# Performance work log

Measured on AMD Instinct MI355X. Metric: run time of the kernel, lower is better.

The kernel has to match this reference:

```python
import jax, jax.numpy as jnp
import numpy as np

NUM_HEADS = 32
NUM_KV_HEADS = 8
HEAD_DIM = 128
SCALE = 1.0 / float(np.sqrt(128.0))
LENS = [1024, 896, 768, 512]          # variable sequence lengths (batch=4)
MAX_SEQLEN = 1024
NUM_SLOTS = 16384                      # 64 blocks * block_size 256
NEG_INF = -1e30


def setup_inputs() -> dict:
    key = jax.random.key(0)
    k0, k1, k2 = jax.random.split(key, 3)
    total = int(sum(LENS))
    q = jax.random.normal(k0, (total, NUM_HEADS, HEAD_DIM), dtype=jnp.float32)
    k = jax.random.normal(k1, (total, NUM_KV_HEADS, HEAD_DIM), dtype=jnp.float32)
    v = jax.random.normal(k2, (total, NUM_KV_HEADS, HEAD_DIM), dtype=jnp.float32)
    k_cache = jnp.zeros((NUM_SLOTS, NUM_KV_HEADS, HEAD_DIM), dtype=jnp.float32)
    v_cache = jnp.zeros((NUM_SLOTS, NUM_KV_HEADS, HEAD_DIM), dtype=jnp.float32)
    slot_mapping = jnp.arange(total, dtype=jnp.int32)
    cu = jnp.concatenate([jnp.zeros((1,), jnp.int32),
                          jnp.cumsum(jnp.array(LENS, dtype=jnp.int32))])
    return {"q": q, "k": k, "v": v, "k_cache": k_cache, "v_cache": v_cache,
            "slot_mapping": slot_mapping, "cu_seqlens_q": cu, "cu_seqlens_k": cu,
            "max_seqlen": MAX_SEQLEN}


def _varlen_prefill_attention(q, k, v, cu_q, cu_k, max_seqlen):
    # q: [T, H, D]; k, v: [T, Hkv, D]; packed variable-length sequences.
    total = q.shape[0]
    B = cu_q.shape[0] - 1
    G = NUM_HEADS // NUM_KV_HEADS  # GQA group size
    lens_q = cu_q[1:] - cu_q[:-1]
    lens_k = cu_k[1:] - cu_k[:-1]
    pos = jnp.arange(max_seqlen)[None, :]                     # [1, S]
    q_idx = jnp.clip(cu_q[:-1, None] + pos, 0, total - 1)     # [B, S]
    k_idx = jnp.clip(cu_k[:-1, None] + pos, 0, total - 1)
    q_valid = pos < lens_q[:, None]                           # [B, S]
    k_valid = pos < lens_k[:, None]
    # Gather into padded [B, S, heads, D] and zero the padding.
    qp = jnp.where(q_valid[:, :, None, None], q[q_idx], 0)
    kp = jnp.where(k_valid[:, :, None, None], k[k_idx], 0)
    vp = jnp.where(k_valid[:, :, None, None], v[k_idx], 0)
    qp = qp.reshape(B, max_seqlen, NUM_KV_HEADS, G, HEAD_DIM)
    # logits: [B, Hkv, G, Sq, Sk]
    logits = jnp.einsum('bqhgd,bkhd->bhgqk', qp, kp) * SCALE
    causal = jnp.arange(max_seqlen)[:, None] >= jnp.arange(max_seqlen)[None, :]
    full_mask = causal[None, :, :] & q_valid[:, :, None] & k_valid[:, None, :]  # [B,Sq,Sk]
    logits = jnp.where(full_mask[:, None, None, :, :], logits, NEG_INF)
    probs = jax.nn.softmax(logits, axis=-1)
    outp = jnp.einsum('bhgqk,bkhd->bqhgd', probs, vp)
    outp = outp.reshape(B, max_seqlen, NUM_HEADS, HEAD_DIM)
    # Scatter padded output back to packed layout.
    dest = q_idx.reshape(-1)
    out_flat = jnp.where(q_valid.reshape(-1)[:, None, None],
                         outp.reshape(-1, NUM_HEADS, HEAD_DIM), 0)
    out = jnp.zeros((total, NUM_HEADS, HEAD_DIM), dtype=q.dtype)
    out = out.at[dest].add(out_flat)
    return out


def reference(q, k, v, k_cache, v_cache, slot_mapping, cu_seqlens_q, cu_seqlens_k, max_seqlen):
    # store_kv_to_cache (scatter into paged cache)
    valid = slot_mapping >= 0
    safe = jnp.where(valid, slot_mapping, 0)
    k_cache_new = k_cache.at[safe].set(k.astype(k_cache.dtype), mode='drop')
    v_cache_new = v_cache.at[safe].set(v.astype(v_cache.dtype), mode='drop')
    # prefill variable-length attention
    out = _varlen_prefill_attention(q, k, v, cu_seqlens_q, cu_seqlens_k, int(max_seqlen))
    return out, k_cache_new, v_cache_new
```

## Files before the change

### kernel.cpp

```cpp
#include <hip/hip_runtime.h>
#include <hip/hip_bf16.h>

#define NUM_HEADS 32
#define NUM_KV 8
#define GQA 4
#define HD 128
#define BM 32
#define BN 64
#define MAXS 1024
#define QTMAX (MAXS / BM)
#define KSTR 136
#define VSTR 72
#define PSTR 72

typedef unsigned short u16;
typedef unsigned int u32;
typedef __attribute__((ext_vector_type(8))) short bf16x8;
typedef __attribute__((ext_vector_type(4))) float f32x4;
typedef __attribute__((ext_vector_type(4))) float f4v;

__device__ __forceinline__ u16 f2bf(float f) {
    __hip_bfloat16 h = __float2bfloat16(f);
    return __builtin_bit_cast(u16, h);
}


__global__ void inv_init(int* __restrict__ inv, int n) {
    int i = blockIdx.x * blockDim.x + threadIdx.x;
    for (; i < n; i += gridDim.x * blockDim.x) inv[i] = -1;
}

__global__ void inv_scatter(const int* __restrict__ slot, int* __restrict__ inv,
                            int total, int nslots) {
    int i = blockIdx.x * blockDim.x + threadIdx.x;
    if (i < total) {
        int s = slot[i];
        if (s >= 0 && s < nslots) inv[s] = i;
    }
}


__global__ __launch_bounds__(256, 2) void fused_kernel(
    const float* __restrict__ q, const float* __restrict__ kk, const float* __restrict__ vv,
    const float* __restrict__ kci, const float* __restrict__ vci,
    const int* __restrict__ inv,
    const int* __restrict__ cu_q, const int* __restrict__ cu_k,
    float* __restrict__ out, float* __restrict__ kco, float* __restrict__ vco,
    int nseq, int nslots, int W, int nattn)
{
    __shared__ __align__(16) u16 Kt[BN * KSTR];
    __shared__ __align__(16) u16 Vt[HD * VSTR];
    __shared__ __align__(16) u16 Pb[4 * 32 * PSTR];

    const int bid = blockIdx.x;
    const int tid = threadIdx.x;

    int u, wid = -1;
    if (bid < 3 * W) {
        int t3 = bid / 3, r3 = bid - 3 * t3;
        if (r3 == 2) { wid = t3; u = -1; }
        else u = t3 * 2 + r3;
    } else {
        u = 2 * W + (bid - 3 * W);
    }

    if (wid >= 0) {
        const f4v* k4   = (const f4v*)kk;
        const f4v* v4   = (const f4v*)vv;
        const f4v* kci4 = (const f4v*)kci;
        const f4v* vci4 = (const f4v*)vci;
        f4v* kco4 = (f4v*)kco;
        f4v* vco4 = (f4v*)vco;
        for (int s = wid; s < nslots; s += W) {
            int t = inv[s];
            size_t so = (size_t)s * 256 + tid;
            f4v kv, vvv;
            if (t >= 0) {
                size_t to = (size_t)t * 256 + tid;
                kv  = k4[to];
                vvv = v4[to];
            } else {
                kv  = __builtin_nontemporal_load(&kci4[so]);
                vvv = __builtin_nontemporal_load(&vci4[so]);
            }
            __builtin_nontemporal_store(kv,  &kco4[so]);
            __builtin_nontemporal_store(vvv, &vco4[so]);
        }
        return;
    }

    if (u >= nattn) return;
    const int per = nseq * NUM_KV;
    const int qt = QTMAX - 1 - u / per;
    const int inner = u % per;
    const int kvh = inner % NUM_KV;
    const int b = inner / NUM_KV;

    const int q0 = cu_q[b];
    const int Lq = cu_q[b + 1] - q0;
    const int k0 = cu_k[b];
    const int Lk = cu_k[b + 1] - k0;
    const int qbase = qt * BM;
    if (qbase >= Lq) return;

    const int wave = tid >> 6;
    const int lane = tid & 63;
    const int c = lane & 15;
    const int quad = lane >> 4;
    const int h = kvh * GQA + wave;

    const float qs = 0.08838834764831845f * 1.44269504088896340f;
    bf16x8 qf[2][4];
#pragma unroll
    for (int rt = 0; rt < 2; ++rt) {
        int row = qbase + rt * 16 + c;
        int tok = q0 + (row < Lq ? row : Lq - 1);
        const float* qp = q + ((size_t)tok * NUM_HEADS + h) * HD + quad * 8;
#pragma unroll
        for (int kc = 0; kc < 4; ++kc) {
            float4 x = *(const float4*)(qp + kc * 32);
            float4 y = *(const float4*)(qp + kc * 32 + 4);
            union { bf16x8 v; u16 s[8]; } uu;
            uu.s[0] = f2bf(x.x * qs); uu.s[1] = f2bf(x.y * qs);
            uu.s[2] = f2bf(x.z * qs); uu.s[3] = f2bf(x.w * qs);
            uu.s[4] = f2bf(y.x * qs); uu.s[5] = f2bf(y.y * qs);
            uu.s[6] = f2bf(y.z * qs); uu.s[7] = f2bf(y.w * qs);
            qf[rt][kc] = uu.v;
        }
    }

    f32x4 Oacc[2][8];
    f32x4 m_i[2], l_i[2];
#pragma unroll
    for (int rt = 0; rt < 2; ++rt) {
        m_i[rt] = (f32x4)(-3.0e38f);
        l_i[rt] = (f32x4)(0.0f);
#pragma unroll
        for (int nt = 0; nt < 8; ++nt) Oacc[rt][nt] = (f32x4)(0.0f);
    }

    const int kmax = min(qbase + BM, Lk);
    const int ntile = (kmax + BN - 1) / BN;

    const int kst_key = tid >> 2;
    const int kst_g   = tid & 3;
    const int vp2     = tid >> 3;
    const int vdg     = tid & 7;
    const int vgran   = vp2 >> 2;
    const int vko     = (vp2 & 3) * 2;

    for (int it = 0; it < ntile; ++it) {
        const int kbase = it * BN;
        __syncthreads();
        {
            int kp = kbase + kst_key;
            int tok = k0 + (kp < Lk ? kp : Lk - 1);
            const float* kg = kk + ((size_t)tok * NUM_KV + kvh) * HD + kst_g * 32;
            u16* krow = &Kt[kst_key * KSTR];
#pragma unroll
            for (int j = 0; j < 4; ++j) {
                float4 x = ((const float4*)kg)[2 * j];
                float4 y = ((const float4*)kg)[2 * j + 1];
                uint4 p;
                p.x = f2bf(x.x) | ((u32)f2bf(x.y) << 16);
                p.y = f2bf(x.z) | ((u32)f2bf(x.w) << 16);
                p.z = f2bf(y.x) | ((u32)f2bf(y.y) << 16);
                p.w = f2bf(y.z) | ((u32)f2bf(y.w) << 16);
                *(uint4*)&krow[(kst_g * 4 + j) * 8] = p;
            }
        }
        {
            int key0 = kbase + 2 * vp2;
            int tok0 = k0 + (key0     < Lk ? key0     : Lk - 1);
            int tok1 = k0 + (key0 + 1 < Lk ? key0 + 1 : Lk - 1);
            const float* va = vv + ((size_t)tok0 * NUM_KV + kvh) * HD + vdg * 16;
            const float* vb = vv + ((size_t)tok1 * NUM_KV + kvh) * HD + vdg * 16;
            int pos = ((vgran + vdg) & 7) * 8 + vko;
#pragma unroll
            for (int i4 = 0; i4 < 4; ++i4) {
                float4 a = ((const float4*)va)[i4];
                float4 bb = ((const float4*)vb)[i4];
                int d0 = vdg * 16 + i4 * 4;
                *(u32*)&Vt[(d0 + 0) * VSTR + pos] = f2bf(a.x) | ((u32)f2bf(bb.x) << 16);
                *(u32*)&Vt[(d0 + 1) * VSTR + pos] = f2bf(a.y) | ((u32)f2bf(bb.y) << 16);
                *(u32*)&Vt[(d0 + 2) * VSTR + pos] = f2bf(a.z) | ((u32)f2bf(bb.z) << 16);
                *(u32*)&Vt[(d0 + 3) * VSTR + pos] = f2bf(a.w) | ((u32)f2bf(bb.w) << 16);
            }
        }
        __syncthreads();

        f32x4 S[2][4];
#pragma unroll
        for (int rt = 0; rt < 2; ++rt)
#pragma unroll
            for (int nt = 0; nt < 4; ++nt) S[rt][nt] = (f32x4)(0.0f);
#pragma unroll
        for (int nt = 0; nt < 4; ++nt) {
            int key = nt * 16 + c;
#pragma unroll
            for (int kc = 0; kc < 4; ++kc) {
                bf16x8 kf = *(const bf16x8*)&Kt[key * KSTR + (kc * 4 + quad) * 8];
                S[0][nt] = __builtin_amdgcn_mfma_f32_16x16x32_bf16(qf[0][kc], kf, S[0][nt], 0, 0, 0);
                S[1][nt] = __builtin_amdgcn_mfma_f32_16x16x32_bf16(qf[1][kc], kf, S[1][nt], 0, 0, 0);
            }
        }

        u16* pb = &Pb[wave * (32 * PSTR)];
#pragma unroll
        for (int rt = 0; rt < 2; ++rt) {
            int rtb = qbase + rt * 16;
            bool notfull = !((kbase + BN <= rtb + 1) && (kbase + BN <= Lk));
            if (notfull) {
                int qp4 = rtb + quad * 4;
#pragma unroll
                for (int nt = 0; nt < 4; ++nt) {
                    int kp = kbase + nt * 16 + c;
                    bool kval = kp < Lk;
#pragma unroll
                    for (int r = 0; r < 4; ++r)
                        if (!(kval && kp <= qp4 + r)) S[rt][nt][r] = -3.0e38f;
                }
            }
            f32x4 rm;
#pragma unroll
            for (int r = 0; r < 4; ++r)
                rm[r] = fmaxf(fmaxf(S[rt][0][r], S[rt][1][r]), fmaxf(S[rt][2][r], S[rt][3][r]));
#pragma unroll
            for (int d2 = 1; d2 < 16; d2 <<= 1)
#pragma unroll
                for (int r = 0; r < 4; ++r)
                    rm[r] = fmaxf(rm[r], __shfl_xor(rm[r], d2));
            f32x4 mn, al;
#pragma unroll
            for (int r = 0; r < 4; ++r) {
                mn[r] = fmaxf(m_i[rt][r], rm[r]);
                al[r] = exp2f(m_i[rt][r] - mn[r]);
            }
            m_i[rt] = mn;
            f32x4 rs = (f32x4)(0.0f);
#pragma unroll
            for (int nt = 0; nt < 4; ++nt)
#pragma unroll
                for (int r = 0; r < 4; ++r) {
                    float p = exp2f(S[rt][nt][r] - mn[r]);
                    S[rt][nt][r] = p;
                    rs[r] += p;
                }
#pragma unroll
            for (int d2 = 1; d2 < 16; d2 <<= 1)
#pragma unroll
                for (int r = 0; r < 4; ++r)
                    rs[r] += __shfl_xor(rs[r], d2);
#pragma unroll
            for (int r = 0; r < 4; ++r)
                l_i[rt][r] = l_i[rt][r] * al[r] + rs[r];
#pragma unroll
            for (int nt = 0; nt < 8; ++nt)
#pragma unroll
                for (int r = 0; r < 4; ++r)
                    Oacc[rt][nt][r] *= al[r];
#pragma unroll
            for (int nt = 0; nt < 4; ++nt)
#pragma unroll
                for (int r = 0; r < 4; ++r)
                    pb[(rt * 16 + quad * 4 + r) * PSTR + nt * 16 + c] = f2bf(S[rt][nt][r]);
        }
        asm volatile("s_waitcnt lgkmcnt(0)" ::: "memory");
        bf16x8 pf[2][2];
#pragma unroll
        for (int rt = 0; rt < 2; ++rt) {
            pf[rt][0] = *(const bf16x8*)&pb[(rt * 16 + c) * PSTR + quad * 8];
            pf[rt][1] = *(const bf16x8*)&pb[(rt * 16 + c) * PSTR + 32 + quad * 8];
        }
        asm volatile("" ::: "memory");

#pragma unroll
        for (int nt = 0; nt < 8; ++nt) {
            int dim = nt * 16 + c;
#pragma unroll
            for (int kc = 0; kc < 2; ++kc) {
                bf16x8 vf = *(const bf16x8*)&Vt[dim * VSTR + (((kc * 4 + quad) + nt) & 7) * 8];
                Oacc[0][nt] = __builtin_amdgcn_mfma_f32_16x16x32_bf16(pf[0][kc], vf, Oacc[0][nt], 0, 0, 0);
                Oacc[1][nt] = __builtin_amdgcn_mfma_f32_16x16x32_bf16(pf[1][kc], vf, Oacc[1][nt], 0, 0, 0);
            }
        }
    }

#pragma unroll
    for (int rt = 0; rt < 2; ++rt) {
        f32x4 li;
#pragma unroll
        for (int r = 0; r < 4; ++r) li[r] = 1.0f / l_i[rt][r];
#pragma unroll
        for (int r = 0; r < 4; ++r) {
            int row = qbase + rt * 16 + quad * 4 + r;
            if (row < Lq) {
                float* op = out + ((size_t)(q0 + row) * NUM_HEADS + h) * HD + c;
#pragma unroll
                for (int nt = 0; nt < 8; ++nt)
                    op[nt * 16] = Oacc[rt][nt][r] * li[r];
            }
        }
    }
}

extern "C" void kernel_launch(void* const* d_in, const int* in_sizes, int n_in,
                              void* d_out, int out_size, void* d_ws, size_t ws_size,
                              hipStream_t stream) {
    const float* q   = (const float*)d_in[0];
    const float* k   = (const float*)d_in[1];
    const float* v   = (const float*)d_in[2];
    const float* kci = (const float*)d_in[3];
    const float* vci = (const float*)d_in[4];
    const int* slot  = (const int*)d_in[5];
    const int* cuq   = (const int*)d_in[6];
    const int* cuk   = (const int*)d_in[7];

    int total  = in_sizes[0] / (NUM_HEADS * HD);
    int nslots = in_sizes[3] / (NUM_KV * HD);
    int nseq   = in_sizes[6] - 1;

    float* out = (float*)d_out;
    float* kco = out + (size_t)total * NUM_HEADS * HD;
    float* vco = kco + (size_t)nslots * NUM_KV * HD;

    int* inv = (int*)d_ws;
    int nattn = QTMAX * nseq * NUM_KV;
    int W = nattn / 2;
    if (W > 512) W = 512;

    inv_init<<<64, 256, 0, stream>>>(inv, nslots);
    inv_scatter<<<(total + 255) / 256, 256, 0, stream>>>(slot, inv, total, nslots);
    fused_kernel<<<nattn + W, 256, 0, stream>>>(q, k, v, kci, vci, inv, cuq, cuk,
                                                out, kco, vco, nseq, nslots, W, nattn);
}
```

Measured before the change: 399.3 us.

## Compute transposed S=K·Qᵀ so P stays in registers for PV MFMA

Swaps MFMA operands so each lane holds one query row's scores, letting softmax row reductions use two shuffles instead of four and feeding P directly from registers into 16x16x16 bf16 MFMAs for the PV product, which removes the per-wave LDS staging buffer and its wait. Output is written as float4 per lane. Dropping the P buffer reduces LDS use, and launch bounds are raised to 3 blocks per CU. The PV step now uses smaller K=16 MFMAs (twice as many instructions), and the tighter register budget from the new launch bound risks spilling.

```diff
diff --git a/kernel.cpp b/kernel.cpp
--- a/kernel.cpp
+++ b/kernel.cpp
@@ -11,11 +11,11 @@
 #define QTMAX (MAXS / BM)
 #define KSTR 136
 #define VSTR 72
-#define PSTR 72
 
 typedef unsigned short u16;
 typedef unsigned int u32;
 typedef __attribute__((ext_vector_type(8))) short bf16x8;
+typedef __attribute__((ext_vector_type(4))) short bf16x4;
 typedef __attribute__((ext_vector_type(4))) float f32x4;
 typedef __attribute__((ext_vector_type(4))) float f4v;
 
@@ -40,7 +40,7 @@
 }
 
 
-__global__ __launch_bounds__(256, 2) void fused_kernel(
+__global__ __launch_bounds__(256, 3) void fused_kernel(
     const float* __restrict__ q, const float* __restrict__ kk, const float* __restrict__ vv,
     const float* __restrict__ kci, const float* __restrict__ vci,
     const int* __restrict__ inv,
@@ -50,7 +50,6 @@
 {
     __shared__ __align__(16) u16 Kt[BN * KSTR];
     __shared__ __align__(16) u16 Vt[HD * VSTR];
-    __shared__ __align__(16) u16 Pb[4 * 32 * PSTR];
 
     const int bid = blockIdx.x;
     const int tid = threadIdx.x;
@@ -130,11 +129,11 @@
     }
 
     f32x4 Oacc[2][8];
-    f32x4 m_i[2], l_i[2];
+    float m_i[2], l_i[2];
 #pragma unroll
     for (int rt = 0; rt < 2; ++rt) {
-        m_i[rt] = (f32x4)(-3.0e38f);
-        l_i[rt] = (f32x4)(0.0f);
+        m_i[rt] = -3.0e38f;
+        l_i[rt] = 0.0f;
 #pragma unroll
         for (int nt = 0; nt < 8; ++nt) Oacc[rt][nt] = (f32x4)(0.0f);
     }
@@ -200,105 +199,86 @@
 #pragma unroll
             for (int kc = 0; kc < 4; ++kc) {
                 bf16x8 kf = *(const bf16x8*)&Kt[key * KSTR + (kc * 4 + quad) * 8];
-                S[0][nt] = __builtin_amdgcn_mfma_f32_16x16x32_bf16(qf[0][kc], kf, S[0][nt], 0, 0, 0);
-                S[1][nt] = __builtin_amdgcn_mfma_f32_16x16x32_bf16(qf[1][kc], kf, S[1][nt], 0, 0, 0);
-            }
-        }
-
-        u16* pb = &Pb[wave * (32 * PSTR)];
+                S[0][nt] = __builtin_amdgcn_mfma_f32_16x16x32_bf16(kf, qf[0][kc], S[0][nt], 0, 0, 0);
+                S[1][nt] = __builtin_amdgcn_mfma_f32_16x16x32_bf16(kf, qf[1][kc], S[1][nt], 0, 0, 0);
+            }
+        }
+
+        bf16x4 pk[2][4];
 #pragma unroll
         for (int rt = 0; rt < 2; ++rt) {
             int rtb = qbase + rt * 16;
+            int qrow_abs = rtb + c;
             bool notfull = !((kbase + BN <= rtb + 1) && (kbase + BN <= Lk));
             if (notfull) {
-                int qp4 = rtb + quad * 4;
 #pragma unroll
                 for (int nt = 0; nt < 4; ++nt) {
-                    int kp = kbase + nt * 16 + c;
-                    bool kval = kp < Lk;
-#pragma unroll
-                    for (int r = 0; r < 4; ++r)
-                        if (!(kval && kp <= qp4 + r)) S[rt][nt][r] = -3.0e38f;
+                    int kb4 = kbase + nt * 16 + quad * 4;
+#pragma unroll
+                    for (int r = 0; r < 4; ++r) {
+                        int key = kb4 + r;
+                        if (!(key <= qrow_abs && key < Lk)) S[rt][nt][r] = -3.0e38f;
+                    }
                 }
             }
-            f32x4 rm;
-#pragma unroll
-            for (int r = 0; r < 4; ++r)
-                rm[r] = fmaxf(fmaxf(S[rt][0][r], S[rt][1][r]), fmaxf(S[rt][2][r], S[rt][3][r]));
-#pragma unroll
-            for (int d2 = 1; d2 < 16; d2 <<= 1)
+            float rm = -3.0e38f;
+#pragma unroll
+            for (int nt = 0; nt < 4; ++nt)
+#pragma unroll
+                for (int r = 0; r < 4; ++r) rm = fmaxf(rm, S[rt][nt][r]);
+            rm = fmaxf(rm, __shfl_xor(rm, 16));
+            rm = fmaxf(rm, __shfl_xor(rm, 32));
+            float mn = fmaxf(m_i[rt], rm);
+            float al = exp2f(m_i[rt] - mn);
+            m_i[rt] = mn;
+            float rs = 0.0f;
+#pragma unroll
+            for (int nt = 0; nt < 4; ++nt) {
+#pragma unroll
+                for (int r = 0; r < 4; ++r) {
+                    float p = exp2f(S[rt][nt][r] - mn);
+                    S[rt][nt][r] = p;
+                    rs += p;
+                }
+                union { bf16x4 v; u16 s[4]; } pu;
+                pu.s[0] = f2bf(S[rt][nt][0]); pu.s[1] = f2bf(S[rt][nt][1]);
+                pu.s[2] = f2bf(S[rt][nt][2]); pu.s[3] = f2bf(S[rt][nt][3]);
+                pk[rt][nt] = pu.v;
+            }
+            rs += __shfl_xor(rs, 16);
+            rs += __shfl_xor(rs, 32);
+            l_i[rt] = l_i[rt] * al + rs;
+#pragma unroll
+            for (int nt = 0; nt < 8; ++nt)
 #pragma unroll
                 for (int r = 0; r < 4; ++r)
-                    rm[r] = fmaxf(rm[r], __shfl_xor(rm[r], d2));
-            f32x4 mn, al;
-#pragma unroll
-            for (int r = 0; r < 4; ++r) {
-                mn[r] = fmaxf(m_i[rt][r], rm[r]);
-                al[r] = exp2f(m_i[rt][r] - mn[r]);
-            }
-            m_i[rt] = mn;
-            f32x4 rs = (f32x4)(0.0f);
-#pragma unroll
-            for (int nt = 0; nt < 4; ++nt)
-#pragma unroll
-                for (int r = 0; r < 4; ++r) {
-                    float p = exp2f(S[rt][nt][r] - mn[r]);
-                    S[rt][nt][r] = p;
-                    rs[r] += p;
-                }
-#pragma unroll
-            for (int d2 = 1; d2 < 16; d2 <<= 1)
-#pragma unroll
-                for (int r = 0; r < 4; ++r)
-                    rs[r] += __shfl_xor(rs[r], d2);
-#pragma unroll
-            for (int r = 0; r < 4; ++r)
-                l_i[rt][r] = l_i[rt][r] * al[r] + rs[r];
-#pragma unroll
-            for (int nt = 0; nt < 8; ++nt)
-#pragma unroll
-                for (int r = 0; r < 4; ++r)
-                    Oacc[rt][nt][r] *= al[r];
-#pragma unroll
-            for (int nt = 0; nt < 4; ++nt)
-#pragma unroll
-                for (int r = 0; r < 4; ++r)
-                    pb[(rt * 16 + quad * 4 + r) * PSTR + nt * 16 + c] = f2bf(S[rt][nt][r]);
-        }
-        asm volatile("s_waitcnt lgkmcnt(0)" ::: "memory");
-        bf16x8 pf[2][2];
-#pragma unroll
-        for (int rt = 0; rt < 2; ++rt) {
-            pf[rt][0] = *(const bf16x8*)&pb[(rt * 16 + c) * PSTR + quad * 8];
-            pf[rt][1] = *(const bf16x8*)&pb[(rt * 16 + c) * PSTR + 32 + quad * 8];
-        }
-        asm volatile("" ::: "memory");
-
-#pragma unroll
-        for (int nt = 0; nt < 8; ++nt) {
-            int dim = nt * 16 + c;
-#pragma unroll
-            for (int kc = 0; kc < 2; ++kc) {
-                bf16x8 vf = *(const bf16x8*)&Vt[dim * VSTR + (((kc * 4 + quad) + nt) & 7) * 8];
-                Oacc[0][nt] = __builtin_amdgcn_mfma_f32_16x16x32_bf16(pf[0][kc], vf, Oacc[0][nt], 0, 0, 0);
-                Oacc[1][nt] = __builtin_amdgcn_mfma_f32_16x16x32_bf16(pf[1][kc], vf, Oacc[1][nt], 0, 0, 0);
+                    Oacc[rt][nt][r] *= al;
+        }
+
+#pragma unroll
+        for (int nt2 = 0; nt2 < 8; ++nt2) {
+            int dim = nt2 * 16 + c;
+#pragma unroll
+            for (int nt = 0; nt < 4; ++nt) {
+                int g = nt * 2 + (quad >> 1);
+                bf16x4 vf = *(const bf16x4*)&Vt[dim * VSTR + ((g + nt2) & 7) * 8 + (quad & 1) * 4];
+                Oacc[0][nt2] = __builtin_amdgcn_mfma_f32_16x16x16bf16_1k(vf, pk[0][nt], Oacc[0][nt2], 0, 0, 0);
+                Oacc[1][nt2] = __builtin_amdgcn_mfma_f32_16x16x16bf16_1k(vf, pk[1][nt], Oacc[1][nt2], 0, 0, 0);
             }
         }
     }
 
 #pragma unroll
     for (int rt = 0; rt < 2; ++rt) {
-        f32x4 li;
-#pragma unroll
-        for (int r = 0; r < 4; ++r) li[r] = 1.0f / l_i[rt][r];
-#pragma unroll
-        for (int r = 0; r < 4; ++r) {
-            int row = qbase + rt * 16 + quad * 4 + r;
-            if (row < Lq) {
-                float* op = out + ((size_t)(q0 + row) * NUM_HEADS + h) * HD + c;
-#pragma unroll
-                for (int nt = 0; nt < 8; ++nt)
-                    op[nt * 16] = Oacc[rt][nt][r] * li[r];
+        float li = 1.0f / l_i[rt];
+        int qrow = qbase + rt * 16 + c;
+        if (qrow < Lq) {
+            float* op = out + ((size_t)(q0 + qrow) * NUM_HEADS + h) * HD + quad * 4;
+#pragma unroll
+            for (int nt2 = 0; nt2 < 8; ++nt2) {
+                f32x4 o = Oacc[rt][nt2];
+                float4 w = make_float4(o[0] * li, o[1] * li, o[2] * li, o[3] * li);
+                *(float4*)(op + nt2 * 16) = w;
             }
         }
     }
```

Measured after the change: 406.5 us. No clear change (+1.8%).
